# Kernel optimization log

Hardware: AMD Instinct MI355X
Metric: run time of the kernel (lower is better)

Reference implementation:

```python
import jax, jax.numpy as jnp
import numpy as np

NODE_TYPES = ('user', 'vn', 'tag', 'staff', 'producer', 'character', 'trait')
N = {'user': 100000, 'vn': 40000, 'tag': 3000, 'staff': 20000, 'producer': 8000, 'character': 60000, 'trait': 3000}
# (src_type, dst_type) per edge type, in HGATConfig.edge_types order
EDGE_TYPES = (('user','vn'), ('vn','user'), ('vn','tag'), ('tag','vn'), ('vn','staff'), ('staff','vn'),
              ('vn','staff'), ('staff','vn'), ('vn','producer'), ('producer','vn'), ('vn','character'),
              ('character','vn'), ('character','trait'), ('trait','character'))
E_COUNTS = (1000000, 1000000, 500000, 500000, 200000, 200000, 200000, 200000, 100000, 100000, 300000, 300000, 400000, 400000)
HID = 128
LAYERS = 3
# number of edge types targeting each node type (HeteroConv aggr='mean' divisor)
NUM_DST = {'user': 1, 'vn': 6, 'tag': 1, 'staff': 2, 'producer': 1, 'character': 2, 'trait': 1}


def _l2norm(x):
    n = jnp.linalg.norm(x, axis=-1, keepdims=True)
    return x / jnp.maximum(n, 1e-12)


def _layernorm(x, g, b):
    m = jnp.mean(x, axis=-1, keepdims=True)
    v = jnp.mean((x - m) ** 2, axis=-1, keepdims=True)
    return (x - m) * jax.lax.rsqrt(v + 1e-5) * g + b


def _forward(xs, Wp, bp, Wl, bl, Wr, ln_g, ln_b, Wu, bu, Wv, bv, eis):
    # input projection per node type
    h = {t: xs[t] @ Wp[i].T + bp[i] for i, t in enumerate(NODE_TYPES)}
    # inverse in-degree per edge type (constant across layers)
    inv_deg = []
    for e, (st, dt) in enumerate(EDGE_TYPES):
        dst = eis[e][1]
        deg = jax.ops.segment_sum(jnp.ones(dst.shape[0], jnp.float32), dst, num_segments=N[dt])
        inv_deg.append(1.0 / jnp.maximum(deg, 1.0))
    for l in range(LAYERS):
        acc = {t: jnp.zeros((N[t], HID), h[t].dtype) for t in NODE_TYPES}
        for e, (st, dt) in enumerate(EDGE_TYPES):
            src, dst = eis[e][0], eis[e][1]
            # SAGEConv: mean-aggregate neighbor feats, then lin_l(agg) + lin_r(root), L2-normalize
            agg = jax.ops.segment_sum(h[st][src], dst, num_segments=N[dt]) * inv_deg[e][:, None]
            out = agg @ Wl[l, e].T + bl[l, e] + h[dt] @ Wr[l, e].T
            acc[dt] = acc[dt] + _l2norm(out)
        new_h = {}
        for i, t in enumerate(NODE_TYPES):
            x = acc[t] / NUM_DST[t] + h[t]  # HeteroConv mean over edge types + residual
            new_h[t] = jax.nn.relu(_layernorm(x, ln_g[l, i], ln_b[l, i]))  # dropout = identity (eval)
        h = new_h
    user_emb = _l2norm(h['user'] @ Wu.T + bu)
    vn_emb = _l2norm(h['vn'] @ Wv.T + bv)
    return user_emb, vn_emb


def setup_inputs() -> dict:
    key = jax.random.key(0)
    ks = iter(jax.random.split(key, 80))
    inp = {}
    for t in NODE_TYPES:
        inp['x_' + t] = jax.random.normal(next(ks), (N[t], HID), jnp.float32)
    for e, (st, dt) in enumerate(EDGE_TYPES):
        src = jax.random.randint(next(ks), (E_COUNTS[e],), 0, N[st], jnp.int32)
        dst = jax.random.randint(next(ks), (E_COUNTS[e],), 0, N[dt], jnp.int32)
        inp['ei_%d' % e] = jnp.stack([src, dst])
    s = 1.0 / np.sqrt(HID)
    inp['Wp'] = jax.random.normal(next(ks), (7, HID, HID), jnp.float32) * s
    inp['bp'] = jnp.zeros((7, HID), jnp.float32)
    inp['Wl'] = jax.random.normal(next(ks), (LAYERS, 14, HID, HID), jnp.float32) * s
    inp['bl'] = jnp.zeros((LAYERS, 14, HID), jnp.float32)
    inp['Wr'] = jax.random.normal(next(ks), (LAYERS, 14, HID, HID), jnp.float32) * s
    inp['ln_g'] = jnp.ones((LAYERS, 7, HID), jnp.float32)
    inp['ln_b'] = jnp.zeros((LAYERS, 7, HID), jnp.float32)
    inp['Wu'] = jax.random.normal(next(ks), (HID, HID), jnp.float32) * s
    inp['bu'] = jnp.zeros((HID,), jnp.float32)
    inp['Wv'] = jax.random.normal(next(ks), (HID, HID), jnp.float32) * s
    inp['bv'] = jnp.zeros((HID,), jnp.float32)
    return inp


def reference(x_user, x_vn, x_tag, x_staff, x_producer, x_character, x_trait,
              ei_0, ei_1, ei_2, ei_3, ei_4, ei_5, ei_6, ei_7, ei_8, ei_9, ei_10, ei_11, ei_12, ei_13,
              Wp, bp, Wl, bl, Wr, ln_g, ln_b, Wu, bu, Wv, bv):
    xs = {'user': x_user, 'vn': x_vn, 'tag': x_tag, 'staff': x_staff,
          'producer': x_producer, 'character': x_character, 'trait': x_trait}
    eis = [ei_0, ei_1, ei_2, ei_3, ei_4, ei_5, ei_6, ei_7, ei_8, ei_9, ei_10, ei_11, ei_12, ei_13]
    return _forward(xs, Wp, bp, Wl, bl, Wr, ln_g, ln_b, Wu, bu, Wv, bv, eis)
```

## Files before the change

kernel.cpp:

```cpp
#include <hip/hip_runtime.h>
#include <math.h>

#define TOTE 5400000
#define TOTN 234000
#define TOTC 514000
#define HID  128

#define NBUK 499
#define NBLK 1024


typedef __attribute__((ext_vector_type(8))) short short8;
typedef __attribute__((ext_vector_type(8))) __bf16 bf16x8;
typedef __attribute__((ext_vector_type(4))) float floatx4;
typedef __attribute__((ext_vector_type(2))) float float2v;

__constant__ int c_EPRE[15]   = {0,1000000,2000000,2500000,3000000,3200000,3400000,3600000,3800000,3900000,4000000,4300000,4600000,5000000,5400000};
__constant__ int c_ECNT[14]   = {1000000,1000000,500000,500000,200000,200000,200000,200000,100000,100000,300000,300000,400000,400000};
__constant__ int c_CNTOFF[14] = {0,40000,140000,143000,183000,203000,243000,263000,303000,311000,351000,411000,451000,454000};
__constant__ int c_CNTN[14]   = {40000,100000,3000,40000,20000,40000,20000,40000,8000,40000,60000,40000,3000,60000};
__constant__ int c_SRCOFF[14] = {0,100000,100000,140000,100000,143000,100000,143000,100000,163000,100000,171000,171000,231000};
__constant__ int c_NODEPRE[8] = {0,100000,140000,143000,163000,171000,231000,234000};
__constant__ int c_BSH[14]   = {9,10,6,10,10,11,10,11,10,11,11,11,6,11};
__constant__ int c_BBASE[15] = {0,79,177,224,264,284,304,324,344,352,372,402,422,469,499};

static __device__ __forceinline__ unsigned short f2bf(float f) {
    unsigned u = __float_as_uint(f);
    u = u + 0x7FFFu + ((u >> 16) & 1u);
    return (unsigned short)(u >> 16);
}
static __device__ __forceinline__ float bf2f(unsigned short s) {
    return __uint_as_float(((unsigned)s) << 16);
}

struct EdgeArgs { const int* ei[14]; };


__global__ __launch_bounds__(256) void hist_k(EdgeArgs a, int* __restrict__ blkHist) {
    __shared__ int h[NBUK];
    int t = threadIdx.x;
    for (int i = t; i < NBUK; i += 256) h[i] = 0;
    __syncthreads();
    const int per = (TOTE + NBLK - 1) / NBLK;
    int s = blockIdx.x * per;
    int eEnd = min(s + per, TOTE);
    for (int g = s + t; g < eEnd; g += 256) {
        int e = 0;
        while (g >= c_EPRE[e + 1]) e++;
        int k = g - c_EPRE[e];
        int dst = a.ei[e][c_ECNT[e] + k];
        atomicAdd(&h[c_BBASE[e] + (dst >> c_BSH[e])], 1);
    }
    __syncthreads();
    for (int i = t; i < NBUK; i += 256) blkHist[(size_t)i * NBLK + blockIdx.x] = h[i];
}

__global__ __launch_bounds__(256) void scan_blk_k(int* __restrict__ blkHist, int* __restrict__ bktCnt) {
    int b = blockIdx.x;
    int* p = blkHist + (size_t)b * NBLK;
    int t = threadIdx.x;
    int4 v = *(int4*)&p[t * 4];
    int s = v.x + v.y + v.z + v.w;
    int lane = t & 63, w = t >> 6;
    __shared__ int wt[4];
    int incl = s;
    #pragma unroll
    for (int d = 1; d < 64; d <<= 1) { int o = __shfl_up(incl, d); if (lane >= d) incl += o; }
    if (lane == 63) wt[w] = incl;
    __syncthreads();
    int wb = 0;
    for (int i = 0; i < w; i++) wb += wt[i];
    int excl = incl - s + wb;
    int4 o;
    o.x = excl; o.y = excl + v.x; o.z = excl + v.x + v.y; o.w = excl + v.x + v.y + v.z;
    *(int4*)&p[t * 4] = o;
    if (t == 255) bktCnt[b] = excl + s;
}

__global__ __launch_bounds__(512) void scans2_k(const int* __restrict__ bktCnt, int* __restrict__ bktEdgeBase) {
    int t = threadIdx.x;
    int v = (t < NBUK) ? bktCnt[t] : 0;
    int lane = t & 63, w = t >> 6;
    __shared__ int wt[8];
    int incl = v;
    #pragma unroll
    for (int d = 1; d < 64; d <<= 1) { int o = __shfl_up(incl, d); if (lane >= d) incl += o; }
    if (lane == 63) wt[w] = incl;
    __syncthreads();
    int wb = 0;
    for (int i = 0; i < w; i++) wb += wt[i];
    int excl = incl - v + wb;
    if (t < NBUK) bktEdgeBase[t] = excl;
    if (t == NBUK - 1) bktEdgeBase[NBUK] = excl + v;
}

__global__ __launch_bounds__(256) void scatter_k(EdgeArgs a, const int* __restrict__ blkHist,
        const int* __restrict__ bktEdgeBase, unsigned* __restrict__ pool) {
    __shared__ int cur[NBUK];
    int t = threadIdx.x;
    for (int i = t; i < NBUK; i += 256)
        cur[i] = bktEdgeBase[i] + blkHist[(size_t)i * NBLK + blockIdx.x];
    __syncthreads();
    const int per = (TOTE + NBLK - 1) / NBLK;
    int s = blockIdx.x * per;
    int eEnd = min(s + per, TOTE);
    for (int g = s + t; g < eEnd; g += 256) {
        int e = 0;
        while (g >= c_EPRE[e + 1]) e++;
        int k = g - c_EPRE[e];
        int src = a.ei[e][k];
        int dst = a.ei[e][c_ECNT[e] + k];
        int sh = c_BSH[e];
        unsigned rec = ((unsigned)(dst & ((1 << sh) - 1)) << 18) | (unsigned)(c_SRCOFF[e] + src);
        int p = atomicAdd(&cur[c_BBASE[e] + (dst >> sh)], 1);
        pool[p] = rec;
    }
}

__global__ __launch_bounds__(256) void csrfill_k(
        const unsigned* __restrict__ pool, const int* __restrict__ bktEdgeBase,
        int* __restrict__ cnt, int* __restrict__ cursor, float* __restrict__ invdeg,
        int* __restrict__ col) {
    __shared__ int hist[2048];
    __shared__ int cur[2048];
    __shared__ int wtot[4];
    __shared__ int wbase[4];
    int b = blockIdx.x;
    int t = threadIdx.x;
    int e = 0;
    while (b >= c_BBASE[e + 1]) e++;
    int lb = b - c_BBASE[e];
    int sh = c_BSH[e];
    int s0t = lb << sh;
    int span = min(1 << sh, c_CNTN[e] - s0t);
    int gs0 = c_CNTOFF[e] + s0t;
    int ebase = bktEdgeBase[b];
    int nrec = bktEdgeBase[b + 1] - ebase;

    for (int i = t; i < span; i += 256) hist[i] = 0;
    __syncthreads();
    for (int i = t; i < nrec; i += 256) atomicAdd(&hist[pool[ebase + i] >> 18], 1);
    __syncthreads();
    int base = t * 8, loc = 0, lv[8];
    #pragma unroll
    for (int i = 0; i < 8; i++) {
        int ii = base + i;
        int v = (ii < span) ? hist[ii] : 0;
        lv[i] = loc; loc += v;
    }
    int lane = t & 63, w = t >> 6;
    int incl = loc;
    #pragma unroll
    for (int d = 1; d < 64; d <<= 1) { int o = __shfl_up(incl, d); if (lane >= d) incl += o; }
    if (lane == 63) wtot[w] = incl;
    __syncthreads();
    if (t == 0) { int s2 = 0; for (int i = 0; i < 4; i++) { wbase[i] = s2; s2 += wtot[i]; } }
    __syncthreads();
    int texcl = incl - loc + wbase[w];
    #pragma unroll
    for (int i = 0; i < 8; i++) {
        int ii = base + i;
        if (ii < span) cur[ii] = texcl + lv[i];
    }
    __syncthreads();
    for (int i = t; i < span; i += 256) {
        int c = hist[i];
        cnt[gs0 + i] = c;
        cursor[gs0 + i] = ebase + cur[i] + c;
        invdeg[gs0 + i] = 1.0f / fmaxf((float)c, 1.0f);
    }
    __syncthreads();
    for (int i = t; i < nrec; i += 256) {
        unsigned rec = pool[ebase + i];
        int p = atomicAdd(&cur[rec >> 18], 1);
        col[ebase + p] = (int)(rec & 0x3FFFFu);
    }
}

struct XArgs { const float* x[7]; };
__global__ __launch_bounds__(256) void convx_k(XArgs a, unsigned short* __restrict__ hbf) {
    int i4 = blockIdx.x * 256 + threadIdx.x;
    if (i4 >= TOTN * 32) return;
    int idx = i4 * 4;
    int t = 0;
    while (idx >= c_NODEPRE[t + 1] * 128) t++;
    float4 v = *(const float4*)&a.x[t][idx - c_NODEPRE[t] * 128];
    uint2 p;
    p.x = (unsigned)f2bf(v.x) | ((unsigned)f2bf(v.y) << 16);
    p.y = (unsigned)f2bf(v.z) | ((unsigned)f2bf(v.w) << 16);
    *(uint2*)&hbf[idx] = p;
}

struct WArgs { const float* Wp; const float* Wl; const float* Wr; const float* Wu; const float* Wv; };
__global__ __launch_bounds__(256) void convw_k(WArgs a, unsigned short* __restrict__ wbf) {
    int i4 = blockIdx.x * 256 + threadIdx.x;
    if (i4 >= 93 * 4096) return;
    int idx = i4 * 4;
    int m = idx >> 14;
    int i = idx & 16383;
    const float* src;
    if (m < 7)       src = a.Wp + (size_t)m * 16384;
    else if (m < 49) src = a.Wl + (size_t)(m - 7) * 16384;
    else if (m < 91) src = a.Wr + (size_t)(m - 49) * 16384;
    else if (m == 91) src = a.Wu;
    else              src = a.Wv;
    float4 v = *(const float4*)&src[i];
    uint2 p;
    p.x = (unsigned)f2bf(v.x) | ((unsigned)f2bf(v.y) << 16);
    p.y = (unsigned)f2bf(v.z) | ((unsigned)f2bf(v.w) << 16);
    *(uint2*)&wbf[idx] = p;
}

#define ACC8v(u) do { \
    v01 += (float2v){__uint_as_float((u).x << 16), __uint_as_float((u).x & 0xFFFF0000u)}; \
    v23 += (float2v){__uint_as_float((u).y << 16), __uint_as_float((u).y & 0xFFFF0000u)}; \
    v45 += (float2v){__uint_as_float((u).z << 16), __uint_as_float((u).z & 0xFFFF0000u)}; \
    v67 += (float2v){__uint_as_float((u).w << 16), __uint_as_float((u).w & 0xFFFF0000u)}; } while (0)

__global__ __launch_bounds__(256) void agg_k(
        const int* __restrict__ cnt, const int* __restrict__ cursor,
        const float* __restrict__ inv_deg, const int* __restrict__ col,
        const unsigned short* __restrict__ hbf, unsigned short* __restrict__ slotb) {
    int row = blockIdx.x * 16 + (threadIdx.x >> 4);
    if (row >= TOTC) return;
    int li = threadIdx.x & 15;
    int nn = cnt[row];
    int rs = cursor[row] - nn;
    const int* cp = col + rs;
    float2v v01 = {0.f, 0.f}, v23 = {0.f, 0.f}, v45 = {0.f, 0.f}, v67 = {0.f, 0.f};
    int j = 0;
    for (; j + 4 <= nn; j += 4) {
        int c0 = cp[j]     << 7;
        int c1 = cp[j + 1] << 7;
        int c2 = cp[j + 2] << 7;
        int c3 = cp[j + 3] << 7;
        uint4 u0 = *(const uint4*)&hbf[c0 + li * 8];
        uint4 u1 = *(const uint4*)&hbf[c1 + li * 8];
        uint4 u2 = *(const uint4*)&hbf[c2 + li * 8];
        uint4 u3 = *(const uint4*)&hbf[c3 + li * 8];
        ACC8v(u0);
        ACC8v(u1);
        ACC8v(u2);
        ACC8v(u3);
    }
    for (; j < nn; j++) {
        int c = cp[j] << 7;
        uint4 u = *(const uint4*)&hbf[c + li * 8];
        ACC8v(u);
    }
    float inv = inv_deg[row];
    float v[8] = {v01.x, v01.y, v23.x, v23.y, v45.x, v45.y, v67.x, v67.y};
    uint4 o;
    o.x = (unsigned)f2bf(v[0] * inv) | ((unsigned)f2bf(v[1] * inv) << 16);
    o.y = (unsigned)f2bf(v[2] * inv) | ((unsigned)f2bf(v[3] * inv) << 16);
    o.z = (unsigned)f2bf(v[4] * inv) | ((unsigned)f2bf(v[5] * inv) << 16);
    o.w = (unsigned)f2bf(v[6] * inv) | ((unsigned)f2bf(v[7] * inv) << 16);
    *(uint4*)&slotb[(size_t)row * HID + li * 8] = o;
}

struct FusArgs {
    int blockPrefix[8];
    int ns[7];
    int a1off[7][6];
    const unsigned short* W1[7][6];
    const unsigned short* W2[7][6];
    const float* bias[7][6];
    int nodepre[7];
    int nrows[7];
    float invnd[7];
};

__global__ __launch_bounds__(256) void fusedln_k(FusArgs g,
        unsigned short* __restrict__ hbf, const unsigned short* __restrict__ slotb,
        const float* __restrict__ ln_g, const float* __restrict__ ln_b, int l) {
    __shared__ short As2[64 * 168];
    __shared__ short A1c[64 * 40];
    __shared__ short W1c[128 * 40];
    __shared__ short W2c[128 * 40];
    int b = blockIdx.x;
    int t = 0;
    while (b >= g.blockPrefix[t + 1]) t++;
    int nrows = g.nrows[t];
    int row0 = (b - g.blockPrefix[t]) * 64;
    int dst0 = g.nodepre[t] + row0;
    int tid = threadIdx.x;
    int w = tid >> 6, lane = tid & 63;
    int q = lane >> 4, m15 = lane & 15;

    {
        const uint4* h4 = (const uint4*)hbf;
        #pragma unroll
        for (int it = 0; it < 4; it++) {
            int c = tid + it * 256;
            int row = c >> 4, kc = c & 15;
            uint4 v = make_uint4(0u, 0u, 0u, 0u);
            if (row0 + row < nrows) v = h4[(size_t)(dst0 + row) * 16 + kc];
            *(uint4*)&As2[row * 168 + (kc >> 2) * 40 + (kc & 3) * 8] = v;
        }
    }

    floatx4 accsum[8];
    #pragma unroll
    for (int bb = 0; bb < 8; bb++) accsum[bb] = (floatx4){0.f, 0.f, 0.f, 0.f};

    int ns = g.ns[t];
    for (int ei = 0; ei < ns; ei++) {
        const uint4* A14 = (const uint4*)(slotb + (size_t)g.a1off[t][ei] * HID);
        const uint4* W14 = (const uint4*)g.W1[t][ei];
        const uint4* W24 = (const uint4*)g.W2[t][ei];
        floatx4 acc[8];
        #pragma unroll
        for (int bb = 0; bb < 8; bb++) acc[bb] = (floatx4){0.f, 0.f, 0.f, 0.f};
        for (int k0 = 0; k0 < 4; k0++) {
            __syncthreads();
            {
                int row = tid >> 2, kc = tid & 3;
                uint4 v = make_uint4(0u, 0u, 0u, 0u);
                if (row0 + row < nrows) v = A14[(size_t)(row0 + row) * 16 + k0 * 4 + kc];
                *(uint4*)&A1c[row * 40 + kc * 8] = v;
            }
            #pragma unroll
            for (int i = 0; i < 2; i++) {
                int idx = tid + i * 256;
                int c = idx >> 2, kc = idx & 3;
                *(uint4*)&W1c[c * 40 + kc * 8] = W14[(size_t)c * 16 + k0 * 4 + kc];
                *(uint4*)&W2c[c * 40 + kc * 8] = W24[(size_t)c * 16 + k0 * 4 + kc];
            }
            __syncthreads();
            bf16x8 a1 = __builtin_bit_cast(bf16x8, *(const short8*)&A1c[(w * 16 + m15) * 40 + q * 8]);
            bf16x8 a2 = __builtin_bit_cast(bf16x8, *(const short8*)&As2[(w * 16 + m15) * 168 + k0 * 40 + q * 8]);
            #pragma unroll
            for (int bb = 0; bb < 8; bb++) {
                bf16x8 w1 = __builtin_bit_cast(bf16x8, *(const short8*)&W1c[(bb * 16 + m15) * 40 + q * 8]);
                bf16x8 w2 = __builtin_bit_cast(bf16x8, *(const short8*)&W2c[(bb * 16 + m15) * 40 + q * 8]);
                acc[bb] = __builtin_amdgcn_mfma_f32_16x16x32_bf16(a1, w1, acc[bb], 0, 0, 0);
                acc[bb] = __builtin_amdgcn_mfma_f32_16x16x32_bf16(a2, w2, acc[bb], 0, 0, 0);
            }
        }
        const float* bias = g.bias[t][ei];
        #pragma unroll
        for (int bb = 0; bb < 8; bb++) {
            float bv = bias[bb * 16 + m15];
            #pragma unroll
            for (int reg = 0; reg < 4; reg++) acc[bb][reg] += bv;
        }
        #pragma unroll
        for (int reg = 0; reg < 4; reg++) {
            float ss = 0.f;
            #pragma unroll
            for (int bb = 0; bb < 8; bb++) ss += acc[bb][reg] * acc[bb][reg];
            ss += __shfl_xor(ss, 1);
            ss += __shfl_xor(ss, 2);
            ss += __shfl_xor(ss, 4);
            ss += __shfl_xor(ss, 8);
            float sc = 1.0f / fmaxf(sqrtf(ss), 1e-12f);
            #pragma unroll
            for (int bb = 0; bb < 8; bb++) accsum[bb][reg] += acc[bb][reg] * sc;
        }
    }

    float invnd = g.invnd[t];
    const float* gg = ln_g + ((size_t)l * 7 + t) * HID;
    const float* bbp = ln_b + ((size_t)l * 7 + t) * HID;
    float gv[8], bv2[8];
    #pragma unroll
    for (int bb = 0; bb < 8; bb++) {
        gv[bb]  = gg[bb * 16 + m15];
        bv2[bb] = bbp[bb * 16 + m15];
    }
    #pragma unroll
    for (int reg = 0; reg < 4; reg++) {
        int lrow = w * 16 + q * 4 + reg;
        float x[8];
        #pragma unroll
        for (int bb = 0; bb < 8; bb++) {
            float resid = bf2f((unsigned short)As2[lrow * 168 + (bb >> 1) * 40 + (bb & 1) * 16 + m15]);
            x[bb] = accsum[bb][reg] * invnd + resid;
        }
        float s = 0.f;
        #pragma unroll
        for (int bb = 0; bb < 8; bb++) s += x[bb];
        s += __shfl_xor(s, 1);
        s += __shfl_xor(s, 2);
        s += __shfl_xor(s, 4);
        s += __shfl_xor(s, 8);
        float mean = s * (1.0f / 128.0f);
        float vs = 0.f;
        #pragma unroll
        for (int bb = 0; bb < 8; bb++) { float d = x[bb] - mean; vs += d * d; }
        vs += __shfl_xor(vs, 1);
        vs += __shfl_xor(vs, 2);
        vs += __shfl_xor(vs, 4);
        vs += __shfl_xor(vs, 8);
        float rstd = rsqrtf(vs * (1.0f / 128.0f) + 1e-5f);
        if (row0 + lrow < nrows) {
            unsigned short* o = hbf + (size_t)(dst0 + lrow) * HID;
            #pragma unroll
            for (int bb = 0; bb < 8; bb++) {
                float y = (x[bb] - mean) * rstd * gv[bb] + bv2[bb];
                o[bb * 16 + m15] = f2bf(fmaxf(y, 0.f));
            }
        }
    }
}

struct GemmArgs {
    int blockPrefix[15];
    const unsigned short* A1[14];
    const unsigned short* W1[14];
    const float* bias[14]; void* out[14];
    int rows[14];
};

template<int MODE>
__global__ __launch_bounds__(256) void gemm_k(GemmArgs g) {
    __shared__ short As[64 * 40];
    __shared__ short Ws[128 * 40];
    int b = blockIdx.x;
    int s = 0;
    while (b >= g.blockPrefix[s + 1]) s++;
    int rows = g.rows[s];
    int row0 = (b - g.blockPrefix[s]) * 64;
    int t = threadIdx.x;
    int w = t >> 6, lane = t & 63;
    int q = lane >> 4, m15 = lane & 15;

    floatx4 acc[8];
    #pragma unroll
    for (int bb = 0; bb < 8; bb++) acc[bb] = (floatx4){0.f, 0.f, 0.f, 0.f};

    const uint4* A4 = (const uint4*)g.A1[s];
    const uint4* W4 = (const uint4*)g.W1[s];
    for (int k0 = 0; k0 < 128; k0 += 32) {
        __syncthreads();
        {
            int row = t >> 2, kc = t & 3;
            uint4 v = make_uint4(0u, 0u, 0u, 0u);
            if (row0 + row < rows) v = A4[(size_t)(row0 + row) * 16 + (k0 >> 3) + kc];
            *(uint4*)&As[row * 40 + kc * 8] = v;
        }
        #pragma unroll
        for (int i = 0; i < 2; i++) {
            int idx = t + i * 256;
            int c = idx >> 2, kc = idx & 3;
            uint4 v = W4[(size_t)c * 16 + (k0 >> 3) + kc];
            *(uint4*)&Ws[c * 40 + kc * 8] = v;
        }
        __syncthreads();
        bf16x8 af = __builtin_bit_cast(bf16x8, *(const short8*)&As[(w * 16 + m15) * 40 + q * 8]);
        #pragma unroll
        for (int bb = 0; bb < 8; bb++) {
            bf16x8 bf = __builtin_bit_cast(bf16x8, *(const short8*)&Ws[(bb * 16 + m15) * 40 + q * 8]);
            acc[bb] = __builtin_amdgcn_mfma_f32_16x16x32_bf16(af, bf, acc[bb], 0, 0, 0);
        }
    }

    const float* bias = g.bias[s];
    #pragma unroll
    for (int bb = 0; bb < 8; bb++) {
        float bv = bias[bb * 16 + m15];
        #pragma unroll
        for (int reg = 0; reg < 4; reg++) acc[bb][reg] += bv;
    }
    if (MODE != 0) {
        #pragma unroll
        for (int reg = 0; reg < 4; reg++) {
            float ss = 0.f;
            #pragma unroll
            for (int bb = 0; bb < 8; bb++) ss += acc[bb][reg] * acc[bb][reg];
            ss += __shfl_xor(ss, 1);
            ss += __shfl_xor(ss, 2);
            ss += __shfl_xor(ss, 4);
            ss += __shfl_xor(ss, 8);
            float sc = 1.0f / fmaxf(sqrtf(ss), 1e-12f);
            #pragma unroll
            for (int bb = 0; bb < 8; bb++) acc[bb][reg] *= sc;
        }
    }
    int rbase = row0 + w * 16 + q * 4;
    if (MODE == 3) {
        float* out = (float*)g.out[s];
        #pragma unroll
        for (int reg = 0; reg < 4; reg++) {
            int r = rbase + reg;
            if (r < rows) {
                float* o = out + (size_t)r * HID;
                #pragma unroll
                for (int bb = 0; bb < 8; bb++) o[bb * 16 + m15] = acc[bb][reg];
            }
        }
    } else {
        unsigned short* out = (unsigned short*)g.out[s];
        #pragma unroll
        for (int reg = 0; reg < 4; reg++) {
            int r = rbase + reg;
            if (r < rows) {
                unsigned short* o = out + (size_t)r * HID;
                #pragma unroll
                for (int bb = 0; bb < 8; bb++) o[bb * 16 + m15] = f2bf(acc[bb][reg]);
            }
        }
    }
}

extern "C" void kernel_launch(void* const* d_in, const int* in_sizes, int n_in,
                              void* d_out, int out_size, void* d_ws, size_t ws_size,
                              hipStream_t stream) {
    (void)in_sizes; (void)n_in; (void)out_size; (void)ws_size;
    const float* Wp   = (const float*)d_in[21];
    const float* bp   = (const float*)d_in[22];
    const float* bl   = (const float*)d_in[24];
    const float* ln_g = (const float*)d_in[26];
    const float* ln_b = (const float*)d_in[27];
    const float* bu   = (const float*)d_in[29];
    const float* bv   = (const float*)d_in[31];
    float* out = (float*)d_out;

    unsigned short* h_bf   = (unsigned short*)d_ws;
    unsigned short* w_bf   = h_bf + (size_t)TOTN * HID;
    unsigned short* slotb  = w_bf + (size_t)93 * 16384;
    int*            cnt    = (int*)(slotb + (size_t)TOTC * HID);
    int*            cursor = cnt + TOTC;
    float*          invdeg = (float*)(cursor + TOTC);
    unsigned*       pool   = (unsigned*)(invdeg + TOTC);
    int*            blkHist = (int*)(pool + (size_t)TOTE);
    int*            ctrl    = blkHist + (size_t)NBUK * NBLK;
    int* bktCnt       = ctrl;
    int* bktEdgeBase  = ctrl + NBUK;

    int* col = (int*)d_out;

    static const int CNTOFF[14] = {0,40000,140000,143000,183000,203000,243000,263000,303000,311000,351000,411000,451000,454000};
    static const int NODEPRE[8] = {0,100000,140000,143000,163000,171000,231000,234000};
    static const int NT[7]      = {100000,40000,3000,20000,8000,60000,3000};
    static const int FEED_NS[7] = {1,6,1,2,1,2,1};
    static const int FEED_E[7][6] = {
        {1,0,0,0,0,0},
        {0,3,5,7,9,11},
        {2,0,0,0,0,0},
        {4,6,0,0,0,0},
        {8,0,0,0,0,0},
        {10,13,0,0,0,0},
        {12,0,0,0,0,0}};
    static const float INVND[7] = {1.0f, 1.0f/6.0f, 1.0f, 0.5f, 1.0f, 0.5f, 1.0f};

    EdgeArgs ea;
    for (int e = 0; e < 14; e++) ea.ei[e] = (const int*)d_in[7 + e];

    hist_k<<<NBLK, 256, 0, stream>>>(ea, blkHist);
    scan_blk_k<<<NBUK, 256, 0, stream>>>(blkHist, bktCnt);
    scans2_k<<<1, 512, 0, stream>>>(bktCnt, bktEdgeBase);
    scatter_k<<<NBLK, 256, 0, stream>>>(ea, blkHist, bktEdgeBase, pool);
    csrfill_k<<<NBUK, 256, 0, stream>>>(pool, bktEdgeBase, cnt, cursor, invdeg, col);

    {
        XArgs xa;
        for (int t = 0; t < 7; t++) xa.x[t] = (const float*)d_in[t];
        convx_k<<<(TOTN * 32 + 255) / 256, 256, 0, stream>>>(xa, h_bf);
        WArgs wa = {Wp, (const float*)d_in[23], (const float*)d_in[25],
                    (const float*)d_in[28], (const float*)d_in[30]};
        convw_k<<<(93 * 4096 + 255) / 256, 256, 0, stream>>>(wa, w_bf);
    }

    {
        GemmArgs ga;
        int pre = 0; ga.blockPrefix[0] = 0;
        for (int t = 0; t < 7; t++) {
            ga.A1[t] = h_bf + (size_t)NODEPRE[t] * HID;
            ga.W1[t] = w_bf + (size_t)t * 16384;
            ga.bias[t] = bp + (size_t)t * HID;
            ga.out[t] = h_bf + (size_t)NODEPRE[t] * HID;
            ga.rows[t] = NT[t];
            pre += (NT[t] + 63) / 64;
            ga.blockPrefix[t + 1] = pre;
        }
        for (int s = 7; s < 14; s++) { ga.blockPrefix[s + 1] = pre; ga.rows[s] = 0; }
        gemm_k<0><<<pre, 256, 0, stream>>>(ga);
    }

    FusArgs fa;
    int fgrid;
    {
        int pre = 0; fa.blockPrefix[0] = 0;
        for (int t = 0; t < 7; t++) {
            fa.ns[t] = FEED_NS[t];
            fa.nodepre[t] = NODEPRE[t];
            fa.nrows[t] = NT[t];
            fa.invnd[t] = INVND[t];
            for (int j = 0; j < 6; j++) fa.a1off[t][j] = CNTOFF[FEED_E[t][j]];
            pre += (NT[t] + 63) / 64;
            fa.blockPrefix[t + 1] = pre;
        }
        fgrid = pre;
    }
    for (int l = 0; l < 3; l++) {
        agg_k<<<(TOTC + 15) / 16, 256, 0, stream>>>(cnt, cursor, invdeg, col, h_bf, slotb);
        for (int t = 0; t < 7; t++) {
            for (int j = 0; j < 6; j++) {
                int e = FEED_E[t][j];
                fa.W1[t][j]   = w_bf + (size_t)(7  + l * 14 + e) * 16384;
                fa.W2[t][j]   = w_bf + (size_t)(49 + l * 14 + e) * 16384;
                fa.bias[t][j] = bl + ((size_t)l * 14 + e) * HID;
            }
        }
        fusedln_k<<<fgrid, 256, 0, stream>>>(fa, h_bf, slotb, ln_g, ln_b, l);
    }

    {
        GemmArgs ga;
        ga.blockPrefix[0] = 0;
        ga.A1[0] = h_bf;
        ga.W1[0] = w_bf + (size_t)91 * 16384;
        ga.bias[0] = bu;                        ga.out[0] = out;
        ga.rows[0] = 100000;
        ga.blockPrefix[1] = (100000 + 63) / 64;
        ga.A1[1] = h_bf + (size_t)100000 * HID;
        ga.W1[1] = w_bf + (size_t)92 * 16384;
        ga.bias[1] = bv;                        ga.out[1] = out + (size_t)100000 * HID;
        ga.rows[1] = 40000;
        int tot = ga.blockPrefix[1] + (40000 + 63) / 64;
        for (int s = 2; s < 14; s++) { ga.blockPrefix[s + 1] = tot; ga.rows[s] = 0; }
        ga.blockPrefix[2] = tot;
        gemm_k<3><<<tot, 256, 0, stream>>>(ga);
    }
}
```

Baseline: 1.345 ms.

## Aggregate 16 rows per 16-lane group with shuffled cooperative index loads

The aggregation kernel now has each 16-lane group walk 16 consecutive destination rows instead of a single row, and the grid shrinks by 16x to match. Neighbor indices are loaded cooperatively, one per lane, and broadcast with wave shuffles instead of every lane reading the same index. The inner loop is unrolled to 8 outstanding row gathers. This aims to cut redundant index loads and raise memory-level parallelism. The cost is fewer waves in flight and per-group serialization across rows with uneven degrees, which may leave load imbalance inside a wave.

```diff
diff --git a/kernel.cpp b/kernel.cpp
--- a/kernel.cpp
+++ b/kernel.cpp
@@ -221,41 +221,58 @@
         const int* __restrict__ cnt, const int* __restrict__ cursor,
         const float* __restrict__ inv_deg, const int* __restrict__ col,
         const unsigned short* __restrict__ hbf, unsigned short* __restrict__ slotb) {
-    int row = blockIdx.x * 16 + (threadIdx.x >> 4);
-    if (row >= TOTC) return;
-    int li = threadIdx.x & 15;
-    int nn = cnt[row];
-    int rs = cursor[row] - nn;
-    const int* cp = col + rs;
-    float2v v01 = {0.f, 0.f}, v23 = {0.f, 0.f}, v45 = {0.f, 0.f}, v67 = {0.f, 0.f};
-    int j = 0;
-    for (; j + 4 <= nn; j += 4) {
-        int c0 = cp[j]     << 7;
-        int c1 = cp[j + 1] << 7;
-        int c2 = cp[j + 2] << 7;
-        int c3 = cp[j + 3] << 7;
-        uint4 u0 = *(const uint4*)&hbf[c0 + li * 8];
-        uint4 u1 = *(const uint4*)&hbf[c1 + li * 8];
-        uint4 u2 = *(const uint4*)&hbf[c2 + li * 8];
-        uint4 u3 = *(const uint4*)&hbf[c3 + li * 8];
-        ACC8v(u0);
-        ACC8v(u1);
-        ACC8v(u2);
-        ACC8v(u3);
-    }
-    for (; j < nn; j++) {
-        int c = cp[j] << 7;
-        uint4 u = *(const uint4*)&hbf[c + li * 8];
-        ACC8v(u);
-    }
-    float inv = inv_deg[row];
-    float v[8] = {v01.x, v01.y, v23.x, v23.y, v45.x, v45.y, v67.x, v67.y};
-    uint4 o;
-    o.x = (unsigned)f2bf(v[0] * inv) | ((unsigned)f2bf(v[1] * inv) << 16);
-    o.y = (unsigned)f2bf(v[2] * inv) | ((unsigned)f2bf(v[3] * inv) << 16);
-    o.z = (unsigned)f2bf(v[4] * inv) | ((unsigned)f2bf(v[5] * inv) << 16);
-    o.w = (unsigned)f2bf(v[6] * inv) | ((unsigned)f2bf(v[7] * inv) << 16);
-    *(uint4*)&slotb[(size_t)row * HID + li * 8] = o;
+    int lane = threadIdx.x & 63;
+    int li = lane & 15;
+    int qb = lane & 48;
+    int q = blockIdx.x * 16 + (threadIdx.x >> 4);
+    int s0 = q * 16;
+    int sEnd = min(s0 + 16, TOTC);
+    for (int row = s0; row < sEnd; row++) {
+        int nn = cnt[row];
+        int rs = cursor[row] - nn;
+        const int* cp = col + rs;
+        float2v v01 = {0.f, 0.f}, v23 = {0.f, 0.f}, v45 = {0.f, 0.f}, v67 = {0.f, 0.f};
+        int j = 0;
+        while (j < nn) {
+            int take = min(nn - j, 16);
+            int cidx = (li < take) ? cp[j + li] : 0;
+            int r = 0;
+            for (; r + 8 <= take; r += 8) {
+                int c0 = __shfl(cidx, qb + r)     << 7;
+                int c1 = __shfl(cidx, qb + r + 1) << 7;
+                int c2 = __shfl(cidx, qb + r + 2) << 7;
+                int c3 = __shfl(cidx, qb + r + 3) << 7;
+                int c4 = __shfl(cidx, qb + r + 4) << 7;
+                int c5 = __shfl(cidx, qb + r + 5) << 7;
+                int c6 = __shfl(cidx, qb + r + 6) << 7;
+                int c7 = __shfl(cidx, qb + r + 7) << 7;
+                uint4 u0 = *(const uint4*)&hbf[c0 + li * 8];
+                uint4 u1 = *(const uint4*)&hbf[c1 + li * 8];
+                uint4 u2 = *(const uint4*)&hbf[c2 + li * 8];
+                uint4 u3 = *(const uint4*)&hbf[c3 + li * 8];
+                uint4 u4 = *(const uint4*)&hbf[c4 + li * 8];
+                uint4 u5 = *(const uint4*)&hbf[c5 + li * 8];
+                uint4 u6 = *(const uint4*)&hbf[c6 + li * 8];
+                uint4 u7 = *(const uint4*)&hbf[c7 + li * 8];
+                ACC8v(u0); ACC8v(u1); ACC8v(u2); ACC8v(u3);
+                ACC8v(u4); ACC8v(u5); ACC8v(u6); ACC8v(u7);
+            }
+            for (; r < take; r++) {
+                int c = __shfl(cidx, qb + r) << 7;
+                uint4 u = *(const uint4*)&hbf[c + li * 8];
+                ACC8v(u);
+            }
+            j += take;
+        }
+        float inv = inv_deg[row];
+        float v[8] = {v01.x, v01.y, v23.x, v23.y, v45.x, v45.y, v67.x, v67.y};
+        uint4 o;
+        o.x = (unsigned)f2bf(v[0] * inv) | ((unsigned)f2bf(v[1] * inv) << 16);
+        o.y = (unsigned)f2bf(v[2] * inv) | ((unsigned)f2bf(v[3] * inv) << 16);
+        o.z = (unsigned)f2bf(v[4] * inv) | ((unsigned)f2bf(v[5] * inv) << 16);
+        o.w = (unsigned)f2bf(v[6] * inv) | ((unsigned)f2bf(v[7] * inv) << 16);
+        *(uint4*)&slotb[(size_t)row * HID + li * 8] = o;
+    }
 }
 
 struct FusArgs {
@@ -594,7 +611,7 @@
         fgrid = pre;
     }
     for (int l = 0; l < 3; l++) {
-        agg_k<<<(TOTC + 15) / 16, 256, 0, stream>>>(cnt, cursor, invdeg, col, h_bf, slotb);
+        agg_k<<<(TOTC + 255) / 256, 256, 0, stream>>>(cnt, cursor, invdeg, col, h_bf, slotb);
         for (int t = 0; t < 7; t++) {
             for (int j = 0; j < 6; j++) {
                 int e = FEED_E[t][j];
```

New measurement: 2.147 ms. 1.6x slower.
